# Optimization experiments

Measured on AMD Instinct MI355X. Metric: run time of the kernel, lower is better.

## Reference

```python
import jax, jax.numpy as jnp
import numpy as np

N = 50000
E = 800000
HEADS = 4
C = 64  # per-head channels
IN = 256
NEG_SLOPE = 0.2


def setup_inputs() -> dict:
    key = jax.random.key(0)
    k = jax.random.split(key, 6)
    x = jax.random.normal(k[0], (N, IN), dtype=jnp.float32)
    edge_index = jax.random.randint(k[1], (2, E), 0, N, dtype=jnp.int64)
    # Glorot-ish scale for weights
    W = jax.random.normal(k[2], (IN, HEADS * C), dtype=jnp.float32) * (1.0 / np.sqrt(IN))
    att_src = jax.random.normal(k[3], (HEADS, C), dtype=jnp.float32) * (1.0 / np.sqrt(C))
    att_dst = jax.random.normal(k[4], (HEADS, C), dtype=jnp.float32) * (1.0 / np.sqrt(C))
    bias = jax.random.normal(k[5], (HEADS * C,), dtype=jnp.float32) * 0.02
    return {"x": x, "edge_index": edge_index, "W": W, "att_src": att_src,
            "att_dst": att_dst, "bias": bias}


def _gat_forward(x, edge_index, W, att_src, att_dst, bias):
    n = x.shape[0]
    h = (x @ W).reshape(n, HEADS, C)  # [N, H, C]

    # add self loops (PyG default add_self_loops=True)
    loop = jnp.arange(n, dtype=edge_index.dtype)
    src = jnp.concatenate([edge_index[0], loop])  # [E+N]
    dst = jnp.concatenate([edge_index[1], loop])

    # per-node attention contributions  [N, H]
    a_src = jnp.einsum('nhc,hc->nh', h, att_src)
    a_dst = jnp.einsum('nhc,hc->nh', h, att_dst)

    # edge logits with leaky relu  [E+N, H]
    logits = a_src[src] + a_dst[dst]
    logits = jnp.where(logits >= 0, logits, NEG_SLOPE * logits)

    # segment softmax over destination neighborhoods
    seg_max = jax.ops.segment_max(logits, dst, num_segments=n)  # [N, H]
    seg_max = jnp.where(jnp.isfinite(seg_max), seg_max, 0.0)
    ex = jnp.exp(logits - seg_max[dst])
    denom = jax.ops.segment_sum(ex, dst, num_segments=n)  # [N, H]
    alpha = ex / (denom[dst] + 1e-16)  # [E+N, H]

    # weighted scatter-add of source messages
    msgs = alpha[:, :, None] * h[src]  # [E+N, H, C]
    out = jax.ops.segment_sum(msgs, dst, num_segments=n)  # [N, H, C]
    out = out.reshape(n, HEADS * C) + bias
    return jax.nn.relu(out)


def reference(x, edge_index, W, att_src, att_dst, bias):
    return _gat_forward(x, edge_index, W, att_src, att_dst, bias)
```

## Files before the change

### kernel.cpp

```cpp
#include <hip/hip_runtime.h>
#include <hip/hip_bf16.h>
#include <math.h>

#define NEG 0.2f
#define BSH 5
#define EPB 2048

typedef __attribute__((ext_vector_type(4))) float f4;
typedef __attribute__((ext_vector_type(8))) short s8;

__device__ __forceinline__ short f2bf(float f) {
    unsigned u = __float_as_uint(f);
    u += 0x7fff + ((u >> 16) & 1);
    return (short)(u >> 16);
}
__device__ __forceinline__ unsigned pk2(float a, float b) {
    union { __hip_bfloat162 h; unsigned u; } c;
    c.h = __float22bfloat162_rn(make_float2(a, b));
    return c.u;
}
__device__ __forceinline__ float bf2f(unsigned short s) {
    return __uint_as_float(((unsigned)s) << 16);
}

__global__ __launch_bounds__(256) void prep_count(
    const float* __restrict__ W, short* __restrict__ Wt, int* __restrict__ off,
    const int* __restrict__ ei, int* __restrict__ hist2d,
    int E, int N, int NBUCK, int NB, int Etot)
{
    const int blk = blockIdx.x, t = threadIdx.x;
    if (blk < 256) {
        int id = blk * 256 + t;
        int n = id >> 8, k = id & 255;
        Wt[id] = f2bf(W[k * 256 + n]);
        if (id == 0) off[N] = Etot;
        return;
    }
    extern __shared__ int lh[];
    const int cblk = blk - 256;
    for (int b = t; b < NBUCK; b += 256) lh[b] = 0;
    __syncthreads();
    const int e0 = cblk * EPB;
    if (e0 + EPB <= E) {
#pragma unroll
        for (int i = 0; i < EPB / 1024; ++i) {
            int e = e0 + i * 1024 + t * 4;
            int4 d = *(const int4*)(ei + E + e);
            atomicAdd(&lh[d.x >> BSH], 1);
            atomicAdd(&lh[d.y >> BSH], 1);
            atomicAdd(&lh[d.z >> BSH], 1);
            atomicAdd(&lh[d.w >> BSH], 1);
        }
    } else {
        for (int i = 0; i < EPB / 256; ++i) {
            int e = e0 + i * 256 + t;
            if (e < Etot) {
                int dte = (e < E) ? ei[E + e] : (e - E);
                atomicAdd(&lh[dte >> BSH], 1);
            }
        }
    }
    __syncthreads();
    for (int b = t; b < NBUCK; b += 256) hist2d[b * NB + cblk] = lh[b];
}

__global__ __launch_bounds__(512) void gemm_attn(
    const float* __restrict__ x, const short* __restrict__ Wt,
    const float* __restrict__ att_src, const float* __restrict__ att_dst,
    short* __restrict__ hb, float* __restrict__ a_src_n,
    float* __restrict__ a_dst_n, int M)
{
    __shared__ __align__(16) short xs[2][128][32];
    const int t = threadIdx.x;
    const int lane = t & 63, wv = t >> 6;
    const int wr = wv >> 2;
    const int hd = wv & 3;
    const int quad = lane >> 4, l15 = lane & 15;
    const int n0 = blockIdx.x * 128;

    const int row = t >> 2, kq = t & 3;
    const bool okr = (n0 + row) < M;
    const float* xp = x + (size_t)(n0 + row) * 256 + kq * 8;

    const short* wbase = Wt + (size_t)(hd * 64 + l15) * 256 + quad * 8;

    f4 acc[4][4];
#pragma unroll
    for (int i = 0; i < 4; ++i)
#pragma unroll
        for (int j = 0; j < 4; ++j) acc[i][j] = (f4)(0.f);

    float4 v0 = {}, v1 = {};
    if (okr) { const float4* p = (const float4*)xp; v0 = p[0]; v1 = p[1]; }

    s8 af[4];
#pragma unroll
    for (int i = 0; i < 4; ++i)
        af[i] = *(const s8*)(wbase + (size_t)(i * 16) * 256);

    int buf = 0;
#pragma unroll
    for (int ks = 0; ks < 8; ++ks) {
        uint4 u = { pk2(v0.x, v0.y), pk2(v0.z, v0.w), pk2(v1.x, v1.y), pk2(v1.z, v1.w) };
        *(uint4*)&xs[buf][row][kq * 8] = u;
        __syncthreads();

        if (ks < 7 && okr) {
            const float4* p = (const float4*)(xp + (ks + 1) * 32);
            v0 = p[0]; v1 = p[1];
        }

        s8 afn[4];
        if (ks < 7) {
#pragma unroll
            for (int i = 0; i < 4; ++i)
                afn[i] = *(const s8*)(wbase + (size_t)(i * 16) * 256 + (ks + 1) * 32);
        }

        s8 bf[4];
#pragma unroll
        for (int j = 0; j < 4; ++j)
            bf[j] = *(const s8*)&xs[buf][wr * 64 + j * 16 + l15][quad * 8];
#pragma unroll
        for (int i = 0; i < 4; ++i)
#pragma unroll
            for (int j = 0; j < 4; ++j)
                acc[i][j] = __builtin_amdgcn_mfma_f32_16x16x32_bf16(af[i], bf[j], acc[i][j], 0, 0, 0);

        if (ks < 7) {
#pragma unroll
            for (int i = 0; i < 4; ++i) af[i] = afn[i];
        }
        buf ^= 1;
    }

    float asv[4][4], adv[4][4];
#pragma unroll
    for (int i = 0; i < 4; ++i)
#pragma unroll
        for (int rr = 0; rr < 4; ++rr) {
            asv[i][rr] = att_src[hd * 64 + i * 16 + quad * 4 + rr];
            adv[i][rr] = att_dst[hd * 64 + i * 16 + quad * 4 + rr];
        }

#pragma unroll
    for (int j = 0; j < 4; ++j) {
        const int node = n0 + wr * 64 + j * 16 + l15;
        const bool ok = node < M;
        float ps = 0.f, pd = 0.f;
#pragma unroll
        for (int i = 0; i < 4; ++i)
#pragma unroll
            for (int rr = 0; rr < 4; ++rr) {
                float v = acc[i][j][rr];
                ps = fmaf(v, asv[i][rr], ps);
                pd = fmaf(v, adv[i][rr], pd);
            }
        ps += __shfl_xor(ps, 16); ps += __shfl_xor(ps, 32);
        pd += __shfl_xor(pd, 16); pd += __shfl_xor(pd, 32);
        if (ok && quad == 0) {
            a_src_n[node * 4 + hd] = ps;
            a_dst_n[node * 4 + hd] = pd;
        }
        if (ok) {
#pragma unroll
            for (int i = 0; i < 4; ++i) {
                uint2 pk = make_uint2(pk2(acc[i][j][0], acc[i][j][1]),
                                      pk2(acc[i][j][2], acc[i][j][3]));
                *(uint2*)&hb[(size_t)node * 256 + hd * 64 + i * 16 + quad * 4] = pk;
            }
        }
    }
}

__global__ __launch_bounds__(1024) void scan1(const int* __restrict__ src,
                                              int* __restrict__ dst,
                                              int* __restrict__ bsum, int Ntot)
{
    __shared__ int wsum[16], wexc[16];
    const int t = threadIdx.x, lane = t & 63, w = t >> 6;
    const int idx = blockIdx.x * 1024 + t;
    int v = (idx < Ntot) ? src[idx] : 0;
    int val = v;
#pragma unroll
    for (int o = 1; o < 64; o <<= 1) {
        int u = __shfl_up(val, o);
        if (lane >= o) val += u;
    }
    if (lane == 63) wsum[w] = val;
    __syncthreads();
    if (t < 16) {
        int s = wsum[t];
#pragma unroll
        for (int o = 1; o < 16; o <<= 1) {
            int u = __shfl_up(s, o, 16);
            if (t >= o) s += u;
        }
        wexc[t] = s - wsum[t];
        if (t == 15) bsum[blockIdx.x] = s;
    }
    __syncthreads();
    if (idx < Ntot) dst[idx] = wexc[w] + val - v;
}

__global__ __launch_bounds__(1024) void scan2v(const int* __restrict__ bsum,
                                               int* __restrict__ bexc, int nb)
{
    __shared__ int wsum[16], wexc[16];
    const int t = threadIdx.x, lane = t & 63, w = t >> 6;
    int v = (t < nb) ? bsum[t] : 0;
    int val = v;
#pragma unroll
    for (int o = 1; o < 64; o <<= 1) {
        int u = __shfl_up(val, o);
        if (lane >= o) val += u;
    }
    if (lane == 63) wsum[w] = val;
    __syncthreads();
    if (t < 16) {
        int s = wsum[t];
#pragma unroll
        for (int o = 1; o < 16; o <<= 1) {
            int u = __shfl_up(s, o, 16);
            if (t >= o) s += u;
        }
        wexc[t] = s - wsum[t];
    }
    __syncthreads();
    if (t < nb) bexc[t] = wexc[w] + val - v;
}

__global__ __launch_bounds__(256) void scatter2(const int* __restrict__ ei,
                                                const int* __restrict__ scanned,
                                                const int* __restrict__ bexc,
                                                unsigned* __restrict__ bucketed,
                                                int E, int N, int NBUCK, int NB)
{
    extern __shared__ int lcur[];
    const int t = threadIdx.x, blk = blockIdx.x;
    for (int b = t; b < NBUCK; b += 256) {
        int idx = b * NB + blk;
        lcur[b] = scanned[idx] + bexc[idx >> 10];
    }
    __syncthreads();
    const int e0 = blk * EPB, Etot = E + N;
    if (e0 + EPB <= E) {
#pragma unroll
        for (int i = 0; i < EPB / 1024; ++i) {
            int e = e0 + i * 1024 + t * 4;
            int4 s4 = *(const int4*)(ei + e);
            int4 d4 = *(const int4*)(ei + E + e);
            int p0 = atomicAdd(&lcur[d4.x >> BSH], 1);
            bucketed[p0] = (unsigned)s4.x | ((unsigned)(d4.x & 31) << 20);
            int p1 = atomicAdd(&lcur[d4.y >> BSH], 1);
            bucketed[p1] = (unsigned)s4.y | ((unsigned)(d4.y & 31) << 20);
            int p2 = atomicAdd(&lcur[d4.z >> BSH], 1);
            bucketed[p2] = (unsigned)s4.z | ((unsigned)(d4.z & 31) << 20);
            int p3 = atomicAdd(&lcur[d4.w >> BSH], 1);
            bucketed[p3] = (unsigned)s4.w | ((unsigned)(d4.w & 31) << 20);
        }
    } else {
        for (int i = 0; i < EPB / 256; ++i) {
            int e = e0 + i * 256 + t;
            if (e < Etot) {
                int src, dte;
                if (e < E) { src = ei[e]; dte = ei[E + e]; }
                else       { src = e - E; dte = src; }
                int pos = atomicAdd(&lcur[dte >> BSH], 1);
                bucketed[pos] = (unsigned)src | ((unsigned)(dte & 31) << 20);
            }
        }
    }
}

__global__ __launch_bounds__(256) void csr_build(
    const unsigned* __restrict__ bucketed, const int* __restrict__ scanned,
    const int* __restrict__ bexc, int* __restrict__ off, int* __restrict__ csr,
    int N, int NB, int NBUCK, int Etot)
{
    __shared__ unsigned est[2048];
    __shared__ int ldeg4[4][32], lcur4[4][32], loff[32];
    const int t = threadIdx.x, wv = t >> 6, b = blockIdx.x;

    const int i0 = b * NB;
    const int gbase = scanned[i0] + bexc[i0 >> 10];
    int gend;
    if (b + 1 == NBUCK) gend = Etot;
    else { int i1 = (b + 1) * NB; gend = scanned[i1] + bexc[i1 >> 10]; }
    int cnt = gend - gbase;
    if (cnt > 2048) cnt = 2048;

    if (t < 128) ldeg4[t >> 5][t & 31] = 0;
    __syncthreads();
    for (int i = t; i < cnt; i += 256) {
        unsigned en = bucketed[gbase + i];
        est[i] = en;
        atomicAdd(&ldeg4[wv][en >> 20], 1);
    }
    __syncthreads();
    if (t < 32) {
        int d0 = ldeg4[0][t], d1 = ldeg4[1][t], d2 = ldeg4[2][t], d3 = ldeg4[3][t];
        int tot = d0 + d1 + d2 + d3;
        int val = tot;
#pragma unroll
        for (int o = 1; o < 32; o <<= 1) {
            int u = __shfl_up(val, o, 32);
            if (t >= o) val += u;
        }
        int excl = val - tot;
        loff[t] = excl;
        lcur4[0][t] = excl;
        lcur4[1][t] = excl + d0;
        lcur4[2][t] = excl + d0 + d1;
        lcur4[3][t] = excl + d0 + d1 + d2;
    }
    __syncthreads();
    for (int i = t; i < cnt; i += 256) {
        unsigned en = est[i];
        int pos = atomicAdd(&lcur4[wv][en >> 20], 1);
        csr[gbase + pos] = (int)(en & 0xFFFFF);
    }
    if (t < 32) {
        int n = (b << BSH) + t;
        if (n < N) off[n] = gbase + loff[t];
    }
}

__global__ __launch_bounds__(256) void aggregate(const short* __restrict__ hb,
                                                 const float* __restrict__ a_src_n,
                                                 const float* __restrict__ a_dst_n,
                                                 const int* __restrict__ off,
                                                 const int* __restrict__ csr,
                                                 const float* __restrict__ bias,
                                                 float* __restrict__ out, int N)
{
    __shared__ float lds_w[4][64][4];
    __shared__ int   lds_s[4][64];
    const int wv = threadIdx.x >> 6;
    const int lane = threadIdx.x & 63;
    const int half = lane >> 5, l31 = lane & 31;
    const int n = blockIdx.x * 4 + wv;
    if (n >= N) return;

    const int base = off[n];
    const int d = off[n + 1] - base;
    const float4 ad = *(const float4*)(a_dst_n + 4 * n);
    const int hl = l31 >> 3;

    float acc[8] = {0.f, 0.f, 0.f, 0.f, 0.f, 0.f, 0.f, 0.f};
    float4 sum = make_float4(0.f, 0.f, 0.f, 0.f);
    const uint4* hp = (const uint4*)hb;

    for (int c0 = 0; c0 < d; c0 += 64) {
        int j = c0 + lane;
        int s = 0;
        float4 w4 = make_float4(0.f, 0.f, 0.f, 0.f);
        if (j < d) {
            s = csr[base + j];
            float4 as = *(const float4*)(a_src_n + 4 * s);
            float lx = as.x + ad.x; lx = lx >= 0.f ? lx : NEG * lx;
            float ly = as.y + ad.y; ly = ly >= 0.f ? ly : NEG * ly;
            float lz = as.z + ad.z; lz = lz >= 0.f ? lz : NEG * lz;
            float lw = as.w + ad.w; lw = lw >= 0.f ? lw : NEG * lw;
            w4 = make_float4(__expf(lx), __expf(ly), __expf(lz), __expf(lw));
        }
        sum.x += w4.x; sum.y += w4.y; sum.z += w4.z; sum.w += w4.w;
        *(float4*)&lds_w[wv][lane][0] = w4;
        lds_s[wv][lane] = s;
        __builtin_amdgcn_wave_barrier();

        const int cl = (d - c0) < 64 ? (d - c0) : 64;
        int jj = 0;
        for (; jj + 4 <= cl; jj += 4) {
            int   s0 = lds_s[wv][jj + half];
            int   s1 = lds_s[wv][jj + 2 + half];
            float w0 = lds_w[wv][jj + half][hl];
            float w1 = lds_w[wv][jj + 2 + half][hl];
            uint4 v0 = hp[(size_t)s0 * 32 + l31];
            uint4 v1 = hp[(size_t)s1 * 32 + l31];
            acc[0] = fmaf(w0, bf2f((unsigned short)(v0.x & 0xffff)), acc[0]);
            acc[1] = fmaf(w0, bf2f((unsigned short)(v0.x >> 16)),    acc[1]);
            acc[2] = fmaf(w0, bf2f((unsigned short)(v0.y & 0xffff)), acc[2]);
            acc[3] = fmaf(w0, bf2f((unsigned short)(v0.y >> 16)),    acc[3]);
            acc[4] = fmaf(w0, bf2f((unsigned short)(v0.z & 0xffff)), acc[4]);
            acc[5] = fmaf(w0, bf2f((unsigned short)(v0.z >> 16)),    acc[5]);
            acc[6] = fmaf(w0, bf2f((unsigned short)(v0.w & 0xffff)), acc[6]);
            acc[7] = fmaf(w0, bf2f((unsigned short)(v0.w >> 16)),    acc[7]);
            acc[0] = fmaf(w1, bf2f((unsigned short)(v1.x & 0xffff)), acc[0]);
            acc[1] = fmaf(w1, bf2f((unsigned short)(v1.x >> 16)),    acc[1]);
            acc[2] = fmaf(w1, bf2f((unsigned short)(v1.y & 0xffff)), acc[2]);
            acc[3] = fmaf(w1, bf2f((unsigned short)(v1.y >> 16)),    acc[3]);
            acc[4] = fmaf(w1, bf2f((unsigned short)(v1.z & 0xffff)), acc[4]);
            acc[5] = fmaf(w1, bf2f((unsigned short)(v1.z >> 16)),    acc[5]);
            acc[6] = fmaf(w1, bf2f((unsigned short)(v1.w & 0xffff)), acc[6]);
            acc[7] = fmaf(w1, bf2f((unsigned short)(v1.w >> 16)),    acc[7]);
        }
        for (; jj < cl; jj += 2) {
            int   s0 = lds_s[wv][jj + half];
            float w0 = lds_w[wv][jj + half][hl];
            uint4 v0 = hp[(size_t)s0 * 32 + l31];
            acc[0] = fmaf(w0, bf2f((unsigned short)(v0.x & 0xffff)), acc[0]);
            acc[1] = fmaf(w0, bf2f((unsigned short)(v0.x >> 16)),    acc[1]);
            acc[2] = fmaf(w0, bf2f((unsigned short)(v0.y & 0xffff)), acc[2]);
            acc[3] = fmaf(w0, bf2f((unsigned short)(v0.y >> 16)),    acc[3]);
            acc[4] = fmaf(w0, bf2f((unsigned short)(v0.z & 0xffff)), acc[4]);
            acc[5] = fmaf(w0, bf2f((unsigned short)(v0.z >> 16)),    acc[5]);
            acc[6] = fmaf(w0, bf2f((unsigned short)(v0.w & 0xffff)), acc[6]);
            acc[7] = fmaf(w0, bf2f((unsigned short)(v0.w >> 16)),    acc[7]);
        }
        __builtin_amdgcn_wave_barrier();
    }

#pragma unroll
    for (int k = 0; k < 8; ++k) acc[k] += __shfl_xor(acc[k], 32);

#pragma unroll
    for (int o = 32; o > 0; o >>= 1) {
        sum.x += __shfl_xor(sum.x, o);
        sum.y += __shfl_xor(sum.y, o);
        sum.z += __shfl_xor(sum.z, o);
        sum.w += __shfl_xor(sum.w, o);
    }
    float sh = (hl & 2) ? ((hl & 1) ? sum.w : sum.z) : ((hl & 1) ? sum.y : sum.x);
    float ih = 1.f / (sh + 1e-16f);

    if (half == 0) {
        const float4* bp = (const float4*)bias + l31 * 2;
        float4 b0 = bp[0], b1 = bp[1];
        float4 o0, o1;
        o0.x = fmaxf(fmaf(acc[0], ih, b0.x), 0.f);
        o0.y = fmaxf(fmaf(acc[1], ih, b0.y), 0.f);
        o0.z = fmaxf(fmaf(acc[2], ih, b0.z), 0.f);
        o0.w = fmaxf(fmaf(acc[3], ih, b0.w), 0.f);
        o1.x = fmaxf(fmaf(acc[4], ih, b1.x), 0.f);
        o1.y = fmaxf(fmaf(acc[5], ih, b1.y), 0.f);
        o1.z = fmaxf(fmaf(acc[6], ih, b1.z), 0.f);
        o1.w = fmaxf(fmaf(acc[7], ih, b1.w), 0.f);
        float4* op = (float4*)(out + (size_t)n * 256) + l31 * 2;
        op[0] = o0;
        op[1] = o1;
    }
}

extern "C" void kernel_launch(void* const* d_in, const int* in_sizes, int n_in,
                              void* d_out, int out_size, void* d_ws, size_t ws_size,
                              hipStream_t stream)
{
    const float* x       = (const float*)d_in[0];
    const int*   ei      = (const int*)d_in[1];
    const float* W       = (const float*)d_in[2];
    const float* att_src = (const float*)d_in[3];
    const float* att_dst = (const float*)d_in[4];
    const float* bias    = (const float*)d_in[5];
    float* out = (float*)d_out;

    const int N = in_sizes[0] / 256;
    const int E = in_sizes[1] / 2;
    const int Etot = E + N;
    const int NBUCK = (N + 31) >> BSH;
    const int NB = (Etot + EPB - 1) / EPB;
    const int Ntot = NBUCK * NB;
    const int nb1 = (Ntot + 1023) / 1024;

    char* p = (char*)d_ws;
    short*    hb      = (short*)p;    p += (size_t)N * 256 * sizeof(short);
    short*    Wt      = (short*)p;    p += 256 * 256 * sizeof(short);
    float*    a_src_n = (float*)p;    p += (size_t)N * 4 * sizeof(float);
    float*    a_dst_n = (float*)p;    p += (size_t)N * 4 * sizeof(float);
    int*      hist2d  = (int*)p;      p += (size_t)Ntot * sizeof(int);
    int*      scanned = (int*)p;      p += (size_t)Ntot * sizeof(int);
    int*      bsum    = (int*)p;      p += 1024 * sizeof(int);
    int*      bexc    = (int*)p;      p += 1024 * sizeof(int);
    int*      off     = (int*)p;      p += (size_t)(N + 1) * sizeof(int);
    unsigned* bucketed= (unsigned*)p; p += (size_t)Etot * sizeof(unsigned);
    int*      csr     = (int*)p;      p += (size_t)Etot * sizeof(int);

    prep_count<<<256 + NB, 256, NBUCK * sizeof(int), stream>>>(
        W, Wt, off, ei, hist2d, E, N, NBUCK, NB, Etot);
    gemm_attn<<<(N + 127) / 128, 512, 0, stream>>>(
        x, Wt, att_src, att_dst, hb, a_src_n, a_dst_n, N);
    scan1<<<nb1, 1024, 0, stream>>>(hist2d, scanned, bsum, Ntot);
    scan2v<<<1, 1024, 0, stream>>>(bsum, bexc, nb1);
    scatter2<<<NB, 256, NBUCK * sizeof(int), stream>>>(ei, scanned, bexc, bucketed,
                                                       E, N, NBUCK, NB);
    csr_build<<<NBUCK, 256, 0, stream>>>(bucketed, scanned, bexc, off, csr,
                                         N, NB, NBUCK, Etot);
    aggregate<<<(N + 3) / 4, 256, 0, stream>>>(hb, a_src_n, a_dst_n, off, csr,
                                               bias, out, N);
}
```

Baseline: 230.0 us.

## Replace bucketed two-pass CSR build with per-node degree atomics and scatter

The two-level bucket histogram, bucketed scatter and per-bucket local sort are replaced by a direct per-node degree count using global atomics. That count is fused into the GEMM kernel prologue so it overlaps with the matmul. The degree array is then prefix-scanned and edges are scattered into the CSR with global atomics on per-node cursors. This drops the csr_build kernel and the intermediate bucketed buffer, at the cost of many more contended global atomics and a scatter that writes to random positions.

```diff
diff --git a/kernel.cpp b/kernel.cpp
--- a/kernel.cpp
+++ b/kernel.cpp
@@ -3,8 +3,6 @@
 #include <math.h>
 
 #define NEG 0.2f
-#define BSH 5
-#define EPB 2048
 
 typedef __attribute__((ext_vector_type(4))) float f4;
 typedef __attribute__((ext_vector_type(8))) short s8;
@@ -23,52 +21,32 @@
     return __uint_as_float(((unsigned)s) << 16);
 }
 
-__global__ __launch_bounds__(256) void prep_count(
-    const float* __restrict__ W, short* __restrict__ Wt, int* __restrict__ off,
-    const int* __restrict__ ei, int* __restrict__ hist2d,
-    int E, int N, int NBUCK, int NB, int Etot)
+__global__ __launch_bounds__(256) void prep(
+    const float* __restrict__ W, short* __restrict__ Wt,
+    int* __restrict__ deg, int N)
 {
     const int blk = blockIdx.x, t = threadIdx.x;
     if (blk < 256) {
         int id = blk * 256 + t;
         int n = id >> 8, k = id & 255;
         Wt[id] = f2bf(W[k * 256 + n]);
-        if (id == 0) off[N] = Etot;
         return;
     }
-    extern __shared__ int lh[];
-    const int cblk = blk - 256;
-    for (int b = t; b < NBUCK; b += 256) lh[b] = 0;
-    __syncthreads();
-    const int e0 = cblk * EPB;
-    if (e0 + EPB <= E) {
-#pragma unroll
-        for (int i = 0; i < EPB / 1024; ++i) {
-            int e = e0 + i * 1024 + t * 4;
-            int4 d = *(const int4*)(ei + E + e);
-            atomicAdd(&lh[d.x >> BSH], 1);
-            atomicAdd(&lh[d.y >> BSH], 1);
-            atomicAdd(&lh[d.z >> BSH], 1);
-            atomicAdd(&lh[d.w >> BSH], 1);
-        }
+    int base = (blk - 256) * 1024 + t * 4;
+    if (base + 3 <= N) {
+        *(int4*)(deg + base) = make_int4(0, 0, 0, 0);
     } else {
-        for (int i = 0; i < EPB / 256; ++i) {
-            int e = e0 + i * 256 + t;
-            if (e < Etot) {
-                int dte = (e < E) ? ei[E + e] : (e - E);
-                atomicAdd(&lh[dte >> BSH], 1);
-            }
-        }
-    }
-    __syncthreads();
-    for (int b = t; b < NBUCK; b += 256) hist2d[b * NB + cblk] = lh[b];
+        for (int k = 0; k < 4; ++k)
+            if (base + k <= N) deg[base + k] = 0;
+    }
 }
 
 __global__ __launch_bounds__(512) void gemm_attn(
     const float* __restrict__ x, const short* __restrict__ Wt,
     const float* __restrict__ att_src, const float* __restrict__ att_dst,
     short* __restrict__ hb, float* __restrict__ a_src_n,
-    float* __restrict__ a_dst_n, int M)
+    float* __restrict__ a_dst_n, int M,
+    const int* __restrict__ ei, int* __restrict__ deg, int E)
 {
     __shared__ __align__(16) short xs[2][128][32];
     const int t = threadIdx.x;
@@ -97,6 +75,22 @@
 #pragma unroll
     for (int i = 0; i < 4; ++i)
         af[i] = *(const s8*)(wbase + (size_t)(i * 16) * 256);
+
+    {
+        const int stride = gridDim.x * 512 * 4;
+        for (int e = (blockIdx.x * 512 + t) * 4; e < E; e += stride) {
+            if (e + 3 < E) {
+                int4 d4 = *(const int4*)(ei + E + e);
+                atomicAdd(&deg[d4.x], 1);
+                atomicAdd(&deg[d4.y], 1);
+                atomicAdd(&deg[d4.z], 1);
+                atomicAdd(&deg[d4.w], 1);
+            } else {
+                for (int k = 0; k < 4; ++k)
+                    if (e + k < E) atomicAdd(&deg[ei[E + e + k]], 1);
+            }
+        }
+    }
 
     int buf = 0;
 #pragma unroll
@@ -174,13 +168,15 @@
 }
 
 __global__ __launch_bounds__(1024) void scan1(const int* __restrict__ src,
-                                              int* __restrict__ dst,
-                                              int* __restrict__ bsum, int Ntot)
+                                              int* __restrict__ off,
+                                              int* __restrict__ cur,
+                                              int* __restrict__ bsum,
+                                              int Ntot, int N)
 {
     __shared__ int wsum[16], wexc[16];
     const int t = threadIdx.x, lane = t & 63, w = t >> 6;
     const int idx = blockIdx.x * 1024 + t;
-    int v = (idx < Ntot) ? src[idx] : 0;
+    int v = (idx < N) ? (src[idx] + 1) : 0;
     int val = v;
 #pragma unroll
     for (int o = 1; o < 64; o <<= 1) {
@@ -200,7 +196,11 @@
         if (t == 15) bsum[blockIdx.x] = s;
     }
     __syncthreads();
-    if (idx < Ntot) dst[idx] = wexc[w] + val - v;
+    if (idx < Ntot) {
+        int e = wexc[w] + val - v;
+        off[idx] = e;
+        cur[idx] = e;
+    }
 }
 
 __global__ __launch_bounds__(1024) void scan2v(const int* __restrict__ bsum,
@@ -230,99 +230,32 @@
     if (t < nb) bexc[t] = wexc[w] + val - v;
 }
 
-__global__ __launch_bounds__(256) void scatter2(const int* __restrict__ ei,
-                                                const int* __restrict__ scanned,
-                                                const int* __restrict__ bexc,
-                                                unsigned* __restrict__ bucketed,
-                                                int E, int N, int NBUCK, int NB)
-{
-    extern __shared__ int lcur[];
-    const int t = threadIdx.x, blk = blockIdx.x;
-    for (int b = t; b < NBUCK; b += 256) {
-        int idx = b * NB + blk;
-        lcur[b] = scanned[idx] + bexc[idx >> 10];
-    }
-    __syncthreads();
-    const int e0 = blk * EPB, Etot = E + N;
-    if (e0 + EPB <= E) {
-#pragma unroll
-        for (int i = 0; i < EPB / 1024; ++i) {
-            int e = e0 + i * 1024 + t * 4;
-            int4 s4 = *(const int4*)(ei + e);
-            int4 d4 = *(const int4*)(ei + E + e);
-            int p0 = atomicAdd(&lcur[d4.x >> BSH], 1);
-            bucketed[p0] = (unsigned)s4.x | ((unsigned)(d4.x & 31) << 20);
-            int p1 = atomicAdd(&lcur[d4.y >> BSH], 1);
-            bucketed[p1] = (unsigned)s4.y | ((unsigned)(d4.y & 31) << 20);
-            int p2 = atomicAdd(&lcur[d4.z >> BSH], 1);
-            bucketed[p2] = (unsigned)s4.z | ((unsigned)(d4.z & 31) << 20);
-            int p3 = atomicAdd(&lcur[d4.w >> BSH], 1);
-            bucketed[p3] = (unsigned)s4.w | ((unsigned)(d4.w & 31) << 20);
-        }
+__global__ __launch_bounds__(256) void scatter_at(const int* __restrict__ ei,
+                                                  int* __restrict__ cur,
+                                                  const int* __restrict__ bexc,
+                                                  int* __restrict__ csr,
+                                                  int E, int Etot)
+{
+    const int e = (blockIdx.x * 256 + threadIdx.x) * 4;
+    if (e + 3 < E) {
+        int4 s4 = *(const int4*)(ei + e);
+        int4 d4 = *(const int4*)(ei + E + e);
+        int p0 = atomicAdd(&cur[d4.x], 1) + bexc[d4.x >> 10];
+        int p1 = atomicAdd(&cur[d4.y], 1) + bexc[d4.y >> 10];
+        int p2 = atomicAdd(&cur[d4.z], 1) + bexc[d4.z >> 10];
+        int p3 = atomicAdd(&cur[d4.w], 1) + bexc[d4.w >> 10];
+        csr[p0] = s4.x; csr[p1] = s4.y; csr[p2] = s4.z; csr[p3] = s4.w;
     } else {
-        for (int i = 0; i < EPB / 256; ++i) {
-            int e = e0 + i * 256 + t;
-            if (e < Etot) {
-                int src, dte;
-                if (e < E) { src = ei[e]; dte = ei[E + e]; }
-                else       { src = e - E; dte = src; }
-                int pos = atomicAdd(&lcur[dte >> BSH], 1);
-                bucketed[pos] = (unsigned)src | ((unsigned)(dte & 31) << 20);
+        for (int k = 0; k < 4; ++k) {
+            int ek = e + k;
+            if (ek < Etot) {
+                int src, dst;
+                if (ek < E) { src = ei[ek]; dst = ei[E + ek]; }
+                else        { src = ek - E; dst = src; }
+                int p = atomicAdd(&cur[dst], 1) + bexc[dst >> 10];
+                csr[p] = src;
             }
         }
-    }
-}
-
-__global__ __launch_bounds__(256) void csr_build(
-    const unsigned* __restrict__ bucketed, const int* __restrict__ scanned,
-    const int* __restrict__ bexc, int* __restrict__ off, int* __restrict__ csr,
-    int N, int NB, int NBUCK, int Etot)
-{
-    __shared__ unsigned est[2048];
-    __shared__ int ldeg4[4][32], lcur4[4][32], loff[32];
-    const int t = threadIdx.x, wv = t >> 6, b = blockIdx.x;
-
-    const int i0 = b * NB;
-    const int gbase = scanned[i0] + bexc[i0 >> 10];
-    int gend;
-    if (b + 1 == NBUCK) gend = Etot;
-    else { int i1 = (b + 1) * NB; gend = scanned[i1] + bexc[i1 >> 10]; }
-    int cnt = gend - gbase;
-    if (cnt > 2048) cnt = 2048;
-
-    if (t < 128) ldeg4[t >> 5][t & 31] = 0;
-    __syncthreads();
-    for (int i = t; i < cnt; i += 256) {
-        unsigned en = bucketed[gbase + i];
-        est[i] = en;
-        atomicAdd(&ldeg4[wv][en >> 20], 1);
-    }
-    __syncthreads();
-    if (t < 32) {
-        int d0 = ldeg4[0][t], d1 = ldeg4[1][t], d2 = ldeg4[2][t], d3 = ldeg4[3][t];
-        int tot = d0 + d1 + d2 + d3;
-        int val = tot;
-#pragma unroll
-        for (int o = 1; o < 32; o <<= 1) {
-            int u = __shfl_up(val, o, 32);
-            if (t >= o) val += u;
-        }
-        int excl = val - tot;
-        loff[t] = excl;
-        lcur4[0][t] = excl;
-        lcur4[1][t] = excl + d0;
-        lcur4[2][t] = excl + d0 + d1;
-        lcur4[3][t] = excl + d0 + d1 + d2;
-    }
-    __syncthreads();
-    for (int i = t; i < cnt; i += 256) {
-        unsigned en = est[i];
-        int pos = atomicAdd(&lcur4[wv][en >> 20], 1);
-        csr[gbase + pos] = (int)(en & 0xFFFFF);
-    }
-    if (t < 32) {
-        int n = (b << BSH) + t;
-        if (n < N) off[n] = gbase + loff[t];
     }
 }
 
@@ -330,6 +263,7 @@
                                                  const float* __restrict__ a_src_n,
                                                  const float* __restrict__ a_dst_n,
                                                  const int* __restrict__ off,
+                                                 const int* __restrict__ bexc,
                                                  const int* __restrict__ csr,
                                                  const float* __restrict__ bias,
                                                  float* __restrict__ out, int N)
@@ -342,8 +276,8 @@
     const int n = blockIdx.x * 4 + wv;
     if (n >= N) return;
 
-    const int base = off[n];
-    const int d = off[n + 1] - base;
+    const int base = off[n] + bexc[n >> 10];
+    const int d = off[n + 1] + bexc[(n + 1) >> 10] - base;
     const float4 ad = *(const float4*)(a_dst_n + 4 * n);
     const int hl = l31 >> 3;
 
@@ -457,34 +391,28 @@
     const int N = in_sizes[0] / 256;
     const int E = in_sizes[1] / 2;
     const int Etot = E + N;
-    const int NBUCK = (N + 31) >> BSH;
-    const int NB = (Etot + EPB - 1) / EPB;
-    const int Ntot = NBUCK * NB;
-    const int nb1 = (Ntot + 1023) / 1024;
+    const int Ntot = N + 1;
+    const int nbs = (Ntot + 1023) / 1024;
+    const int nzb = (Ntot + 1023) / 1024;
 
     char* p = (char*)d_ws;
     short*    hb      = (short*)p;    p += (size_t)N * 256 * sizeof(short);
     short*    Wt      = (short*)p;    p += 256 * 256 * sizeof(short);
     float*    a_src_n = (float*)p;    p += (size_t)N * 4 * sizeof(float);
     float*    a_dst_n = (float*)p;    p += (size_t)N * 4 * sizeof(float);
-    int*      hist2d  = (int*)p;      p += (size_t)Ntot * sizeof(int);
-    int*      scanned = (int*)p;      p += (size_t)Ntot * sizeof(int);
+    int*      deg     = (int*)p;      p += (size_t)Ntot * sizeof(int);
+    int*      off     = (int*)p;      p += (size_t)Ntot * sizeof(int);
+    int*      cur     = (int*)p;      p += (size_t)Ntot * sizeof(int);
     int*      bsum    = (int*)p;      p += 1024 * sizeof(int);
     int*      bexc    = (int*)p;      p += 1024 * sizeof(int);
-    int*      off     = (int*)p;      p += (size_t)(N + 1) * sizeof(int);
-    unsigned* bucketed= (unsigned*)p; p += (size_t)Etot * sizeof(unsigned);
     int*      csr     = (int*)p;      p += (size_t)Etot * sizeof(int);
 
-    prep_count<<<256 + NB, 256, NBUCK * sizeof(int), stream>>>(
-        W, Wt, off, ei, hist2d, E, N, NBUCK, NB, Etot);
+    prep<<<256 + nzb, 256, 0, stream>>>(W, Wt, deg, N);
     gemm_attn<<<(N + 127) / 128, 512, 0, stream>>>(
-        x, Wt, att_src, att_dst, hb, a_src_n, a_dst_n, N);
-    scan1<<<nb1, 1024, 0, stream>>>(hist2d, scanned, bsum, Ntot);
-    scan2v<<<1, 1024, 0, stream>>>(bsum, bexc, nb1);
-    scatter2<<<NB, 256, NBUCK * sizeof(int), stream>>>(ei, scanned, bexc, bucketed,
-                                                       E, N, NBUCK, NB);
-    csr_build<<<NBUCK, 256, 0, stream>>>(bucketed, scanned, bexc, off, csr,
-                                         N, NB, NBUCK, Etot);
-    aggregate<<<(N + 3) / 4, 256, 0, stream>>>(hb, a_src_n, a_dst_n, off, csr,
+        x, Wt, att_src, att_dst, hb, a_src_n, a_dst_n, N, ei, deg, E);
+    scan1<<<nbs, 1024, 0, stream>>>(deg, off, cur, bsum, Ntot, N);
+    scan2v<<<1, 1024, 0, stream>>>(bsum, bexc, nbs);
+    scatter_at<<<(Etot + 1023) / 1024, 256, 0, stream>>>(ei, cur, bexc, csr, E, Etot);
+    aggregate<<<(N + 3) / 4, 256, 0, stream>>>(hb, a_src_n, a_dst_n, off, bexc, csr,
                                                bias, out, N);
 }
```

Measured after the change: 273.6 us. 1.19x slower.
